# Kernel tuning notes

Measured on AMD Instinct MI355X. Metric: run time of the kernel, lower is better.

The kernel has to match this reference:

```python
import jax, jax.numpy as jnp
import numpy as np

D, S, O, T, B = 32, 8, 4, 256, 1024  # hidden dim, sensory dim, output dim, steps, batch


def setup_inputs() -> dict:
    key = jax.random.key(0)
    ks = iter(jax.random.split(key, 48))

    def w(*shape):
        # stand-in for orthogonal init scaled to max-abs ~0.99
        return jax.random.normal(next(ks), shape, jnp.float32) * 0.17

    inp = {"obs": jax.random.normal(next(ks), (T, B, S), jnp.float32)}
    inp["enc_w"] = w(D, S)
    inp["enc_b"] = jnp.zeros((D,), jnp.float32)
    for name in ["wW", "wI", "wA", "zW", "zI", "zA", "rW", "rI", "rA",
                 "hW", "hI", "hA", "aW", "aI", "aA"]:
        inp[name] = w(D, D)
    for name in ["att", "wmg", "img", "amg"]:
        inp[name + "_w"] = w(D, 2 * D)
        inp[name + "_b"] = jnp.zeros((D,), jnp.float32)
    inp["z_b"] = -jnp.ones((D,), jnp.float32)  # nn.init.constant_(I_z_bias, -1.0)
    inp["r_b"] = jnp.zeros((D,), jnp.float32)
    inp["h_b"] = jnp.zeros((D,), jnp.float32)
    inp["a_b"] = jnp.zeros((D,), jnp.float32)
    inp["phi_w"] = w(O, D)
    inp["phi_b"] = jnp.zeros((O,), jnp.float32)
    return inp


def reference(obs, enc_w, enc_b, wW, wI, wA, att_w, att_b, wmg_w, wmg_b,
              zW, zI, zA, z_b, rW, rI, rA, r_b, hW, hI, hA, h_b,
              img_w, img_b, aW, aI, aA, a_b, amg_w, amg_b, phi_w, phi_b):
    b, d = obs.shape[1], wW.shape[0]

    def lin(x, w, bias=None):
        y = x @ w.T
        return y + bias if bias is not None else y

    def step(carry, o_t):
        W, I, A = carry
        obs_enc = jnp.tanh(lin(o_t, enc_w, enc_b))
        W_all = lin(W, wW) + lin(I, wI) + lin(A, wA)
        attn = jax.nn.sigmoid(lin(jnp.concatenate([W, I], -1), att_w, att_b))
        mult = jax.nn.sigmoid(lin(jnp.concatenate([I, A], -1), wmg_w, wmg_b))
        W_new = jnp.tanh(obs_enc * attn + W_all * mult)
        z = jax.nn.sigmoid(lin(W_new, zW) + lin(I, zI) + lin(A, zA) + z_b)
        r = jax.nn.sigmoid(lin(W_new, rW) + lin(I, rI) + lin(A, rA) + r_b)
        h = jnp.tanh(lin(W_new, hW) + lin(r * I, hI) + lin(A, hA) + h_b)
        mult_I = jax.nn.sigmoid(lin(jnp.concatenate([W_new, A], -1), img_w, img_b))
        I_new = (1 - z) * I + z * (h * mult_I)
        A_all = lin(W_new, aW) + lin(I_new, aI) + lin(A, aA) + a_b
        mult_A = jax.nn.sigmoid(lin(jnp.concatenate([W_new, I_new], -1), amg_w, amg_b))
        A_new = jnp.tanh(A_all * mult_A)
        return (W_new, I_new, A_new), lin(A_new, phi_w, phi_b)

    z0 = jnp.zeros((b, d), obs.dtype)
    _, actions = jax.lax.scan(step, (z0, z0, z0), obs)
    return actions  # [T, B, O]
```

## Files before the change

kernel.cpp:

```cpp
#include <hip/hip_runtime.h>
#include <hip/hip_bf16.h>

typedef __attribute__((ext_vector_type(4))) float f32x4;
typedef __attribute__((ext_vector_type(8))) short s16x8;
typedef __attribute__((ext_vector_type(2))) unsigned int u32x2;
typedef __attribute__((ext_vector_type(4))) unsigned int u32x4;

#define DEV static __device__ __forceinline__

constexpr int Tn = 256, Bn = 1024, Sn = 8;
constexpr float L2E   =  1.44269504f;
constexpr float NL2E  = -1.44269504f;
constexpr float N2L2E = -2.88539008f;

struct Params {
  const float* obs; const float* enc_w; const float* enc_b;
  const float* mw[15];
  const float* gw[4];
  const float* gb[4];
  const float* z_b; const float* r_b; const float* h_b; const float* a_b;
  const float* phi_w; const float* phi_b;
  float* out;
};

DEV f32x4 ld4(const float* p) { return *(const f32x4*)p; }
DEV f32x4 zero4() { f32x4 r = {0.f,0.f,0.f,0.f}; return r; }
DEV s16x8 zero8() { s16x8 r = {0,0,0,0,0,0,0,0}; return r; }

DEV unsigned cvtpk(float a, float b) {
  __hip_bfloat162 t = __float22bfloat162_rn(make_float2(a, b));
  unsigned u; __builtin_memcpy(&u, &t, 4);
  return u;
}

DEV s16x8 pk2s(f32x4 a, f32x4 b, float s) {
  u32x4 f;
  f[0] = cvtpk(a[0]*s, a[1]*s); f[1] = cvtpk(a[2]*s, a[3]*s);
  f[2] = cvtpk(b[0]*s, b[1]*s); f[3] = cvtpk(b[2]*s, b[3]*s);
  s16x8 r; __builtin_memcpy(&r, &f, 16);
  return r;
}

DEV s16x8 wfrag(const float* w, int row, int ldk, int kofs, int h, float s) {
  const float* p = w + row*ldk + kofs + 4*h;
  return pk2s(ld4(p), ld4(p+16), s);
}

DEV f32x4 MF(s16x8 a, s16x8 b, f32x4 c) {
  return __builtin_amdgcn_mfma_f32_16x16x32_bf16(a, b, c, 0, 0, 0);
}

DEV float ex2(float x)  { return __builtin_amdgcn_exp2f(x); }
DEV float rcp_(float x) { return __builtin_amdgcn_rcpf(x); }
DEV float sg(float a) { return rcp_(1.f + ex2(a)); }
DEV float th(float a) { return fmaf(rcp_(1.f + ex2(a)), 2.f, -1.f); }

DEV unsigned long long pack64(u32x2 v) {
  return ((unsigned long long)v[1] << 32) | v[0];
}
DEV u32x2 unpack64(unsigned long long x) {
  u32x2 r; r[0] = (unsigned)x; r[1] = (unsigned)(x >> 32); return r;
}
DEV u32x2 pkx(f32x4 v) {
  u32x2 r; r[0] = cvtpk(v[0], v[1]); r[1] = cvtpk(v[2], v[3]); return r;
}
DEV s16x8 frag(u32x2 own, u32x2 oth, int wv) {
  u32x4 f;
  if (wv == 0) { f[0]=own[0]; f[1]=own[1]; f[2]=oth[0]; f[3]=oth[1]; }
  else         { f[0]=oth[0]; f[1]=oth[1]; f[2]=own[0]; f[3]=own[1]; }
  s16x8 r; __builtin_memcpy(&r, &f, 16);
  return r;
}

DEV f32x4 scl4(f32x4 v, float s) { f32x4 r; r[0]=v[0]*s; r[1]=v[1]*s; r[2]=v[2]*s; r[3]=v[3]*s; return r; }

__global__ __launch_bounds__(128, 1) void anima_kernel(Params P) {
  const int tid  = threadIdx.x;
  const int wv   = tid >> 6;
  const int lane = tid & 63;
  const int h = lane >> 4, c = lane & 15;
  const int bbase = blockIdx.x * 16;
  const int row = wv*16 + c;

  __shared__ unsigned long long xb[4][128];

  const float msc[15] = {N2L2E,N2L2E,N2L2E,  NL2E,NL2E,NL2E,  NL2E,NL2E,NL2E,
                         N2L2E,N2L2E,N2L2E,  N2L2E,N2L2E,N2L2E};
  s16x8 m[15];
#pragma unroll
  for (int i = 0; i < 15; ++i) m[i] = wfrag(P.mw[i], row, 32, 0, h, msc[i]);

  s16x8 g[4][2];
#pragma unroll
  for (int i = 0; i < 4; ++i)
#pragma unroll
    for (int q = 0; q < 2; ++q)
      g[i][q] = wfrag(P.gw[i], row, 64, 32*q, h, NL2E);

  s16x8 ef = zero8();
  if (h < 2) { f32x4 v = ld4(P.enc_w + row*Sn + 4*h); ef = pk2s(v, zero4(), N2L2E); }

  s16x8 pf = (wv == 0 && c < 4) ? wfrag(P.phi_w, c, 32, 0, h, 1.0f) : zero8();

  const int o = wv*16 + 4*h;
  f32x4 bE  = scl4(ld4(P.enc_b + o), N2L2E);
  f32x4 bAt = scl4(ld4(P.gb[0] + o), NL2E);
  f32x4 bMu = scl4(ld4(P.gb[1] + o), NL2E);
  f32x4 bMI = scl4(ld4(P.gb[2] + o), NL2E);
  f32x4 bMA = scl4(ld4(P.gb[3] + o), NL2E);
  f32x4 bZ  = scl4(ld4(P.z_b + o),  NL2E);
  f32x4 bR  = scl4(ld4(P.r_b + o),  NL2E);
  f32x4 bH  = scl4(ld4(P.h_b + o),  N2L2E);
  f32x4 bA  = scl4(ld4(P.a_b + o),  N2L2E);
  f32x4 pb  = (wv == 0 && h == 0) ? ld4(P.phi_b) : zero4();

  f32x4 iv = zero4();
  s16x8 Wf = zero8(), If = zero8(), Af = zero8();

  f32x4 ob = zero4();
  if (h < 2) ob = ld4(P.obs + (size_t)(bbase + c) * Sn + 4*h);

#pragma unroll 1
  for (int t = 0; t < Tn; ++t) {
    s16x8 Of = (h < 2) ? pk2s(ob, zero4(), 1.0f) : zero8();
    f32x4 nb = ob;
    if (h < 2 && t + 1 < Tn)
      nb = ld4(P.obs + ((size_t)(t+1)*Bn + bbase + c) * Sn + 4*h);

    f32x4 x = MF(m[0], Wf, zero4()); x = MF(m[1], If, x); f32x4 aWl = MF(m[2], Af, x);
    f32x4 y = MF(g[0][0], Wf, bAt);  f32x4 aAt = MF(g[0][1], If, y);
    f32x4 u = MF(g[1][0], If, bMu);  f32x4 aMu = MF(g[1][1], Af, u);
    f32x4 aE = MF(ef, Of, bE);
    f32x4 wn;
#pragma unroll
    for (int r = 0; r < 4; ++r) {
      float etp = fmaf(rcp_(1.f + ex2(aE[r])), -4.f*L2E, 2.f*L2E);
      float at  = sg(aAt[r]);
      float mg  = sg(aMu[r]);
      float wp  = fmaf(etp, at, aWl[r]*mg);
      wn[r] = th(wp);
    }
    u32x2 wn2 = pkx(wn);
    xb[0][tid] = pack64(wn2); __syncthreads();
    s16x8 Wnf = frag(wn2, unpack64(xb[0][tid ^ 64]), wv);

    x = MF(m[3], Wnf, bZ); x = MF(m[4], If, x); f32x4 aZ = MF(m[5], Af, x);
    y = MF(m[6], Wnf, bR); y = MF(m[7], If, y); f32x4 aR = MF(m[8], Af, y);
    u = MF(g[2][0], Wnf, bMI); f32x4 aMI = MF(g[2][1], Af, u);
    f32x4 zz, ri, mi;
#pragma unroll
    for (int r = 0; r < 4; ++r) {
      zz[r] = sg(aZ[r]);
      ri[r] = sg(aR[r]) * iv[r];
      mi[r] = sg(aMI[r]);
    }
    u32x2 ri2 = pkx(ri);
    xb[1][tid] = pack64(ri2); __syncthreads();
    s16x8 rIf = frag(ri2, unpack64(xb[1][tid ^ 64]), wv);

    x = MF(m[9], Wnf, bH); x = MF(m[10], rIf, x); f32x4 aH = MF(m[11], Af, x);
    f32x4 inw;
#pragma unroll
    for (int r = 0; r < 4; ++r) {
      float hv = th(aH[r]);
      float tt = hv * mi[r];
      inw[r] = fmaf(zz[r], tt - iv[r], iv[r]);
    }
    u32x2 in2 = pkx(inw);
    xb[2][tid] = pack64(in2); __syncthreads();
    s16x8 Inf = frag(in2, unpack64(xb[2][tid ^ 64]), wv);

    x = MF(m[12], Wnf, bA); x = MF(m[13], Inf, x); f32x4 aAl = MF(m[14], Af, x);
    y = MF(g[3][0], Wnf, bMA); f32x4 aMA = MF(g[3][1], Inf, y);
    f32x4 an;
#pragma unroll
    for (int r = 0; r < 4; ++r) {
      float ma = sg(aMA[r]);
      an[r] = th(aAl[r] * ma);
    }
    u32x2 an2 = pkx(an);
    xb[3][tid] = pack64(an2); __syncthreads();
    s16x8 Anf = frag(an2, unpack64(xb[3][tid ^ 64]), wv);

    if (wv == 0) {
      f32x4 aP = MF(pf, Anf, pb);
      if (h == 0)
        *(f32x4*)(P.out + ((size_t)t*Bn + bbase + c) * 4) = aP;
    }

    Wf = Wnf; If = Inf; Af = Anf; iv = inw; ob = nb;
  }
}

extern "C" void kernel_launch(void* const* d_in, const int* in_sizes, int n_in,
                              void* d_out, int out_size, void* d_ws, size_t ws_size,
                              hipStream_t stream) {
  (void)in_sizes; (void)n_in; (void)d_ws; (void)ws_size; (void)out_size;
  Params p;
  p.obs   = (const float*)d_in[0];
  p.enc_w = (const float*)d_in[1];
  p.enc_b = (const float*)d_in[2];
  for (int i = 0; i < 15; ++i) p.mw[i] = (const float*)d_in[3 + i];
  for (int i = 0; i < 4; ++i) {
    p.gw[i] = (const float*)d_in[18 + 2*i];
    p.gb[i] = (const float*)d_in[19 + 2*i];
  }
  p.z_b   = (const float*)d_in[26];
  p.r_b   = (const float*)d_in[27];
  p.h_b   = (const float*)d_in[28];
  p.a_b   = (const float*)d_in[29];
  p.phi_w = (const float*)d_in[30];
  p.phi_b = (const float*)d_in[31];
  p.out   = (float*)d_out;

  hipLaunchKernelGGL(anima_kernel, dim3(Bn / 16), dim3(128), 0, stream, p);
}
```

Before: 412.3 us.

## Interleave two batch tiles per block to overlap independent recurrence chains

Each block now processes two independent 16-row batch tiles and interleaves their MFMA chains and activations within every phase, sharing the four barriers per step. The goal is to hide MFMA and transcendental latency in the serial recurrence through instruction-level parallelism. It halves the number of blocks, leaving more CUs idle, and doubles the register state per thread.

```diff
diff --git a/kernel.cpp b/kernel.cpp
--- a/kernel.cpp
+++ b/kernel.cpp
@@ -79,10 +79,10 @@
   const int wv   = tid >> 6;
   const int lane = tid & 63;
   const int h = lane >> 4, c = lane & 15;
-  const int bbase = blockIdx.x * 16;
+  const int bbase = blockIdx.x * 32;
   const int row = wv*16 + c;
 
-  __shared__ unsigned long long xb[4][128];
+  __shared__ unsigned long long xb[4][2][128];
 
   const float msc[15] = {N2L2E,N2L2E,N2L2E,  NL2E,NL2E,NL2E,  NL2E,NL2E,NL2E,
                          N2L2E,N2L2E,N2L2E,  N2L2E,N2L2E,N2L2E};
@@ -114,81 +114,141 @@
   f32x4 bA  = scl4(ld4(P.a_b + o),  N2L2E);
   f32x4 pb  = (wv == 0 && h == 0) ? ld4(P.phi_b) : zero4();
 
-  f32x4 iv = zero4();
-  s16x8 Wf = zero8(), If = zero8(), Af = zero8();
-
-  f32x4 ob = zero4();
-  if (h < 2) ob = ld4(P.obs + (size_t)(bbase + c) * Sn + 4*h);
+  f32x4 iv[2]; s16x8 Wf[2], If[2], Af[2]; f32x4 ob[2];
+#pragma unroll
+  for (int q = 0; q < 2; ++q) {
+    iv[q] = zero4(); Wf[q] = zero8(); If[q] = zero8(); Af[q] = zero8();
+    ob[q] = zero4();
+    if (h < 2) ob[q] = ld4(P.obs + (size_t)(bbase + q*16 + c) * Sn + 4*h);
+  }
 
 #pragma unroll 1
   for (int t = 0; t < Tn; ++t) {
-    s16x8 Of = (h < 2) ? pk2s(ob, zero4(), 1.0f) : zero8();
-    f32x4 nb = ob;
-    if (h < 2 && t + 1 < Tn)
-      nb = ld4(P.obs + ((size_t)(t+1)*Bn + bbase + c) * Sn + 4*h);
-
-    f32x4 x = MF(m[0], Wf, zero4()); x = MF(m[1], If, x); f32x4 aWl = MF(m[2], Af, x);
-    f32x4 y = MF(g[0][0], Wf, bAt);  f32x4 aAt = MF(g[0][1], If, y);
-    f32x4 u = MF(g[1][0], If, bMu);  f32x4 aMu = MF(g[1][1], Af, u);
-    f32x4 aE = MF(ef, Of, bE);
-    f32x4 wn;
-#pragma unroll
-    for (int r = 0; r < 4; ++r) {
-      float etp = fmaf(rcp_(1.f + ex2(aE[r])), -4.f*L2E, 2.f*L2E);
-      float at  = sg(aAt[r]);
-      float mg  = sg(aMu[r]);
-      float wp  = fmaf(etp, at, aWl[r]*mg);
-      wn[r] = th(wp);
-    }
-    u32x2 wn2 = pkx(wn);
-    xb[0][tid] = pack64(wn2); __syncthreads();
-    s16x8 Wnf = frag(wn2, unpack64(xb[0][tid ^ 64]), wv);
-
-    x = MF(m[3], Wnf, bZ); x = MF(m[4], If, x); f32x4 aZ = MF(m[5], Af, x);
-    y = MF(m[6], Wnf, bR); y = MF(m[7], If, y); f32x4 aR = MF(m[8], Af, y);
-    u = MF(g[2][0], Wnf, bMI); f32x4 aMI = MF(g[2][1], Af, u);
-    f32x4 zz, ri, mi;
-#pragma unroll
-    for (int r = 0; r < 4; ++r) {
-      zz[r] = sg(aZ[r]);
-      ri[r] = sg(aR[r]) * iv[r];
-      mi[r] = sg(aMI[r]);
-    }
-    u32x2 ri2 = pkx(ri);
-    xb[1][tid] = pack64(ri2); __syncthreads();
-    s16x8 rIf = frag(ri2, unpack64(xb[1][tid ^ 64]), wv);
-
-    x = MF(m[9], Wnf, bH); x = MF(m[10], rIf, x); f32x4 aH = MF(m[11], Af, x);
-    f32x4 inw;
-#pragma unroll
-    for (int r = 0; r < 4; ++r) {
-      float hv = th(aH[r]);
-      float tt = hv * mi[r];
-      inw[r] = fmaf(zz[r], tt - iv[r], iv[r]);
-    }
-    u32x2 in2 = pkx(inw);
-    xb[2][tid] = pack64(in2); __syncthreads();
-    s16x8 Inf = frag(in2, unpack64(xb[2][tid ^ 64]), wv);
-
-    x = MF(m[12], Wnf, bA); x = MF(m[13], Inf, x); f32x4 aAl = MF(m[14], Af, x);
-    y = MF(g[3][0], Wnf, bMA); f32x4 aMA = MF(g[3][1], Inf, y);
-    f32x4 an;
-#pragma unroll
-    for (int r = 0; r < 4; ++r) {
-      float ma = sg(aMA[r]);
-      an[r] = th(aAl[r] * ma);
-    }
-    u32x2 an2 = pkx(an);
-    xb[3][tid] = pack64(an2); __syncthreads();
-    s16x8 Anf = frag(an2, unpack64(xb[3][tid ^ 64]), wv);
+    s16x8 Of[2]; f32x4 nb[2];
+#pragma unroll
+    for (int q = 0; q < 2; ++q) {
+      Of[q] = (h < 2) ? pk2s(ob[q], zero4(), 1.0f) : zero8();
+      nb[q] = ob[q];
+      if (h < 2 && t + 1 < Tn)
+        nb[q] = ld4(P.obs + ((size_t)(t+1)*Bn + bbase + q*16 + c) * Sn + 4*h);
+    }
+
+    s16x8 Wnf[2];
+    {
+      f32x4 aWl[2], aAt[2], aMu[2], aE[2];
+#pragma unroll
+      for (int q = 0; q < 2; ++q) {
+        f32x4 x = MF(m[0], Wf[q], zero4()); x = MF(m[1], If[q], x); aWl[q] = MF(m[2], Af[q], x);
+        f32x4 y = MF(g[0][0], Wf[q], bAt);  aAt[q] = MF(g[0][1], If[q], y);
+        f32x4 u = MF(g[1][0], If[q], bMu);  aMu[q] = MF(g[1][1], Af[q], u);
+        aE[q]  = MF(ef, Of[q], bE);
+      }
+      u32x2 wn2[2];
+#pragma unroll
+      for (int q = 0; q < 2; ++q) {
+        f32x4 wn;
+#pragma unroll
+        for (int r = 0; r < 4; ++r) {
+          float etp = fmaf(rcp_(1.f + ex2(aE[q][r])), -4.f*L2E, 2.f*L2E);
+          float at  = sg(aAt[q][r]);
+          float mg  = sg(aMu[q][r]);
+          float wp  = fmaf(etp, at, aWl[q][r]*mg);
+          wn[r] = th(wp);
+        }
+        wn2[q] = pkx(wn);
+        xb[0][q][tid] = pack64(wn2[q]);
+      }
+      __syncthreads();
+#pragma unroll
+      for (int q = 0; q < 2; ++q) Wnf[q] = frag(wn2[q], unpack64(xb[0][q][tid ^ 64]), wv);
+    }
+
+    f32x4 zz[2], mi[2]; s16x8 rIf[2];
+    {
+      f32x4 aZ[2], aR[2], aMI[2];
+#pragma unroll
+      for (int q = 0; q < 2; ++q) {
+        f32x4 x = MF(m[3], Wnf[q], bZ); x = MF(m[4], If[q], x); aZ[q] = MF(m[5], Af[q], x);
+        f32x4 y = MF(m[6], Wnf[q], bR); y = MF(m[7], If[q], y); aR[q] = MF(m[8], Af[q], y);
+        f32x4 u = MF(g[2][0], Wnf[q], bMI); aMI[q] = MF(g[2][1], Af[q], u);
+      }
+      u32x2 ri2[2];
+#pragma unroll
+      for (int q = 0; q < 2; ++q) {
+        f32x4 ri;
+#pragma unroll
+        for (int r = 0; r < 4; ++r) {
+          zz[q][r] = sg(aZ[q][r]);
+          ri[r]    = sg(aR[q][r]) * iv[q][r];
+          mi[q][r] = sg(aMI[q][r]);
+        }
+        ri2[q] = pkx(ri);
+        xb[1][q][tid] = pack64(ri2[q]);
+      }
+      __syncthreads();
+#pragma unroll
+      for (int q = 0; q < 2; ++q) rIf[q] = frag(ri2[q], unpack64(xb[1][q][tid ^ 64]), wv);
+    }
+
+    f32x4 inw[2]; s16x8 Inf[2];
+    {
+      f32x4 aH[2];
+#pragma unroll
+      for (int q = 0; q < 2; ++q) {
+        f32x4 x = MF(m[9], Wnf[q], bH); x = MF(m[10], rIf[q], x); aH[q] = MF(m[11], Af[q], x);
+      }
+      u32x2 in2[2];
+#pragma unroll
+      for (int q = 0; q < 2; ++q) {
+#pragma unroll
+        for (int r = 0; r < 4; ++r) {
+          float hv = th(aH[q][r]);
+          float tt = hv * mi[q][r];
+          inw[q][r] = fmaf(zz[q][r], tt - iv[q][r], iv[q][r]);
+        }
+        in2[q] = pkx(inw[q]);
+        xb[2][q][tid] = pack64(in2[q]);
+      }
+      __syncthreads();
+#pragma unroll
+      for (int q = 0; q < 2; ++q) Inf[q] = frag(in2[q], unpack64(xb[2][q][tid ^ 64]), wv);
+    }
+
+    s16x8 Anf[2];
+    {
+      f32x4 aAl[2], aMA[2];
+#pragma unroll
+      for (int q = 0; q < 2; ++q) {
+        f32x4 x = MF(m[12], Wnf[q], bA); x = MF(m[13], Inf[q], x); aAl[q] = MF(m[14], Af[q], x);
+        f32x4 y = MF(g[3][0], Wnf[q], bMA); aMA[q] = MF(g[3][1], Inf[q], y);
+      }
+      u32x2 an2[2];
+#pragma unroll
+      for (int q = 0; q < 2; ++q) {
+        f32x4 an;
+#pragma unroll
+        for (int r = 0; r < 4; ++r) an[r] = th(aAl[q][r] * sg(aMA[q][r]));
+        an2[q] = pkx(an);
+        xb[3][q][tid] = pack64(an2[q]);
+      }
+      __syncthreads();
+#pragma unroll
+      for (int q = 0; q < 2; ++q) Anf[q] = frag(an2[q], unpack64(xb[3][q][tid ^ 64]), wv);
+    }
 
     if (wv == 0) {
-      f32x4 aP = MF(pf, Anf, pb);
-      if (h == 0)
-        *(f32x4*)(P.out + ((size_t)t*Bn + bbase + c) * 4) = aP;
-    }
-
-    Wf = Wnf; If = Inf; Af = Anf; iv = inw; ob = nb;
+#pragma unroll
+      for (int q = 0; q < 2; ++q) {
+        f32x4 aP = MF(pf, Anf[q], pb);
+        if (h == 0)
+          *(f32x4*)(P.out + ((size_t)t*Bn + bbase + q*16 + c) * 4) = aP;
+      }
+    }
+
+#pragma unroll
+    for (int q = 0; q < 2; ++q) {
+      Wf[q] = Wnf[q]; If[q] = Inf[q]; Af[q] = Anf[q]; iv[q] = inw[q]; ob[q] = nb[q];
+    }
   }
 }
 
@@ -213,5 +273,5 @@
   p.phi_b = (const float*)d_in[31];
   p.out   = (float*)d_out;
 
-  hipLaunchKernelGGL(anima_kernel, dim3(Bn / 16), dim3(128), 0, stream, p);
-}
+  hipLaunchKernelGGL(anima_kernel, dim3(Bn / 32), dim3(128), 0, stream, p);
+}
```

After: 636.6 us. 1.54x slower.

## Reorder recurrent step so MFMAs on ready operands overlap barrier exchanges

Applied to the files above, without the earlier changes.

Restructures the time loop so partial matrix products whose inputs are already known (terms on A, I, W_new) are issued before the shared-memory exchange completes and before the fragment is rebuilt. Work for the next step's W-gate products is hoisted into the tail of the current step, and the output projection is deferred to the following iteration. Observation loads are prefetched two steps ahead. The aim is to shorten the serial dependency chain per step by hiding MFMA latency behind barriers, at the cost of more live registers and a peeled final output.

```diff
diff --git a/kernel.cpp b/kernel.cpp
--- a/kernel.cpp
+++ b/kernel.cpp
@@ -115,38 +115,51 @@
   f32x4 pb  = (wv == 0 && h == 0) ? ld4(P.phi_b) : zero4();
 
   f32x4 iv = zero4();
-  s16x8 Wf = zero8(), If = zero8(), Af = zero8();
-
-  f32x4 ob = zero4();
-  if (h < 2) ob = ld4(P.obs + (size_t)(bbase + c) * Sn + 4*h);
+  s16x8 Inf = zero8();
+  u32x2 an2; an2[0] = 0u; an2[1] = 0u;
+
+  f32x4 ob = zero4(), obN = zero4();
+  if (h < 2) ob  = ld4(P.obs + (size_t)(bbase + c) * Sn + 4*h);
+  if (h < 2) obN = ld4(P.obs + ((size_t)1*Bn + bbase + c) * Sn + 4*h);
+  s16x8 Of = (h < 2) ? pk2s(ob, zero4(), 1.0f) : zero8();
+
+  f32x4 tA1 = zero4();
+  f32x4 yAt = bAt;
+  f32x4 uMu = bMu;
+  f32x4 aE  = MF(ef, Of, bE);
+
+  xb[3][tid] = pack64(an2);
+  __syncthreads();
+  unsigned long long pw3 = xb[3][tid ^ 64];
 
 #pragma unroll 1
   for (int t = 0; t < Tn; ++t) {
-    s16x8 Of = (h < 2) ? pk2s(ob, zero4(), 1.0f) : zero8();
-    f32x4 nb = ob;
-    if (h < 2 && t + 1 < Tn)
-      nb = ld4(P.obs + ((size_t)(t+1)*Bn + bbase + c) * Sn + 4*h);
-
-    f32x4 x = MF(m[0], Wf, zero4()); x = MF(m[1], If, x); f32x4 aWl = MF(m[2], Af, x);
-    f32x4 y = MF(g[0][0], Wf, bAt);  f32x4 aAt = MF(g[0][1], If, y);
-    f32x4 u = MF(g[1][0], If, bMu);  f32x4 aMu = MF(g[1][1], Af, u);
-    f32x4 aE = MF(ef, Of, bE);
+    s16x8 Anf = frag(an2, unpack64(pw3), wv);
+    if (wv == 0 && t) {
+      f32x4 aP = MF(pf, Anf, pb);
+      if (h == 0) *(f32x4*)(P.out + ((size_t)(t-1)*Bn + bbase + c) * 4) = aP;
+    }
+    f32x4 aWl = MF(m[2], Anf, tA1);
+    f32x4 aMu = MF(g[1][1], Anf, uMu);
     f32x4 wn;
 #pragma unroll
     for (int r = 0; r < 4; ++r) {
       float etp = fmaf(rcp_(1.f + ex2(aE[r])), -4.f*L2E, 2.f*L2E);
-      float at  = sg(aAt[r]);
+      float at  = sg(yAt[r]);
       float mg  = sg(aMu[r]);
-      float wp  = fmaf(etp, at, aWl[r]*mg);
-      wn[r] = th(wp);
+      wn[r] = th(fmaf(etp, at, aWl[r]*mg));
     }
     u32x2 wn2 = pkx(wn);
-    xb[0][tid] = pack64(wn2); __syncthreads();
-    s16x8 Wnf = frag(wn2, unpack64(xb[0][tid ^ 64]), wv);
-
-    x = MF(m[3], Wnf, bZ); x = MF(m[4], If, x); f32x4 aZ = MF(m[5], Af, x);
-    y = MF(m[6], Wnf, bR); y = MF(m[7], If, y); f32x4 aR = MF(m[8], Af, y);
-    u = MF(g[2][0], Wnf, bMI); f32x4 aMI = MF(g[2][1], Af, u);
+    xb[0][tid] = pack64(wn2);
+    __syncthreads();
+    unsigned long long pw0 = xb[0][tid ^ 64];
+    f32x4 eZ  = MF(m[5], Anf, MF(m[4], Inf, bZ));
+    f32x4 eR  = MF(m[8], Anf, MF(m[7], Inf, bR));
+    f32x4 eMI = MF(g[2][1], Anf, bMI);
+    s16x8 Wnew = frag(wn2, unpack64(pw0), wv);
+    f32x4 aZ  = MF(m[3], Wnew, eZ);
+    f32x4 aR  = MF(m[6], Wnew, eR);
+    f32x4 aMI = MF(g[2][0], Wnew, eMI);
     f32x4 zz, ri, mi;
 #pragma unroll
     for (int r = 0; r < 4; ++r) {
@@ -155,40 +168,50 @@
       mi[r] = sg(aMI[r]);
     }
     u32x2 ri2 = pkx(ri);
-    xb[1][tid] = pack64(ri2); __syncthreads();
-    s16x8 rIf = frag(ri2, unpack64(xb[1][tid ^ 64]), wv);
-
-    x = MF(m[9], Wnf, bH); x = MF(m[10], rIf, x); f32x4 aH = MF(m[11], Af, x);
+    xb[1][tid] = pack64(ri2);
+    __syncthreads();
+    unsigned long long pw1 = xb[1][tid ^ 64];
+    f32x4 eH  = MF(m[11], Anf, MF(m[9],  Wnew, bH));
+    f32x4 eAl = MF(m[14], Anf, MF(m[12], Wnew, bA));
+    f32x4 eMA = MF(g[3][0], Wnew, bMA);
+    s16x8 rIf = frag(ri2, unpack64(pw1), wv);
+    f32x4 aH = MF(m[10], rIf, eH);
     f32x4 inw;
 #pragma unroll
     for (int r = 0; r < 4; ++r) {
       float hv = th(aH[r]);
-      float tt = hv * mi[r];
-      inw[r] = fmaf(zz[r], tt - iv[r], iv[r]);
+      inw[r] = fmaf(zz[r], hv * mi[r] - iv[r], iv[r]);
     }
     u32x2 in2 = pkx(inw);
-    xb[2][tid] = pack64(in2); __syncthreads();
-    s16x8 Inf = frag(in2, unpack64(xb[2][tid ^ 64]), wv);
-
-    x = MF(m[12], Wnf, bA); x = MF(m[13], Inf, x); f32x4 aAl = MF(m[14], Af, x);
-    y = MF(g[3][0], Wnf, bMA); f32x4 aMA = MF(g[3][1], Inf, y);
+    xb[2][tid] = pack64(in2);
+    __syncthreads();
+    unsigned long long pw2 = xb[2][tid ^ 64];
+    f32x4 t0 = MF(m[0], Wnew, zero4());
+    f32x4 y0 = MF(g[0][0], Wnew, bAt);
+    s16x8 OfN = (h < 2) ? pk2s(obN, zero4(), 1.0f) : zero8();
+    aE = MF(ef, OfN, bE);
+    s16x8 Inew = frag(in2, unpack64(pw2), wv);
+    f32x4 aAl = MF(m[13], Inew, eAl);
+    f32x4 aMA = MF(g[3][1], Inew, eMA);
     f32x4 an;
 #pragma unroll
-    for (int r = 0; r < 4; ++r) {
-      float ma = sg(aMA[r]);
-      an[r] = th(aAl[r] * ma);
-    }
-    u32x2 an2 = pkx(an);
-    xb[3][tid] = pack64(an2); __syncthreads();
-    s16x8 Anf = frag(an2, unpack64(xb[3][tid ^ 64]), wv);
-
-    if (wv == 0) {
-      f32x4 aP = MF(pf, Anf, pb);
-      if (h == 0)
-        *(f32x4*)(P.out + ((size_t)t*Bn + bbase + c) * 4) = aP;
-    }
-
-    Wf = Wnf; If = Inf; Af = Anf; iv = inw; ob = nb;
+    for (int r = 0; r < 4; ++r) an[r] = th(aAl[r] * sg(aMA[r]));
+    an2 = pkx(an);
+    xb[3][tid] = pack64(an2);
+    __syncthreads();
+    pw3 = xb[3][tid ^ 64];
+    tA1 = MF(m[1], Inew, t0);
+    yAt = MF(g[0][1], Inew, y0);
+    uMu = MF(g[1][0], Inew, bMu);
+    if (h < 2 && t + 2 < Tn)
+      obN = ld4(P.obs + ((size_t)(t+2)*Bn + bbase + c) * Sn + 4*h);
+    Inf = Inew; iv = inw;
+  }
+
+  s16x8 Anf = frag(an2, unpack64(pw3), wv);
+  if (wv == 0) {
+    f32x4 aP = MF(pf, Anf, pb);
+    if (h == 0) *(f32x4*)(P.out + ((size_t)(Tn-1)*Bn + bbase + c) * 4) = aP;
   }
 }
 
```

Result: faster. 390.2 us (-5.4%).

## Interleave two batch tiles per block and hoist off-critical-path MFMAs across barriers

Applied to the files above, without the earlier changes.

Each block now processes two independent 16-row batch tiles (A and B) in the same instruction stream, so their MFMA and transcendental chains can fill each other's latency bubbles, and the grid is halved. MFMA terms that do not depend on the freshly exchanged fragment are issued before it is read from shared memory, and next-step partial products, obs encodings and the phi output are moved across iterations as software pipelining. This trades more register pressure and half as many blocks (32 instead of 64, less CU parallelism) for shorter dependent latency per step.

```diff
diff --git a/kernel.cpp b/kernel.cpp
--- a/kernel.cpp
+++ b/kernel.cpp
@@ -79,10 +79,10 @@
   const int wv   = tid >> 6;
   const int lane = tid & 63;
   const int h = lane >> 4, c = lane & 15;
-  const int bbase = blockIdx.x * 16;
+  const int bbase = blockIdx.x * 32;
   const int row = wv*16 + c;
 
-  __shared__ unsigned long long xb[4][128];
+  __shared__ unsigned long long xb[4][2][128];
 
   const float msc[15] = {N2L2E,N2L2E,N2L2E,  NL2E,NL2E,NL2E,  NL2E,NL2E,NL2E,
                          N2L2E,N2L2E,N2L2E,  N2L2E,N2L2E,N2L2E};
@@ -114,81 +114,171 @@
   f32x4 bA  = scl4(ld4(P.a_b + o),  N2L2E);
   f32x4 pb  = (wv == 0 && h == 0) ? ld4(P.phi_b) : zero4();
 
-  f32x4 iv = zero4();
-  s16x8 Wf = zero8(), If = zero8(), Af = zero8();
-
-  f32x4 ob = zero4();
-  if (h < 2) ob = ld4(P.obs + (size_t)(bbase + c) * Sn + 4*h);
+  f32x4 ivA = zero4(), ivB = zero4();
+  s16x8 InfA = zero8(), InfB = zero8();
+  u32x2 an2A; an2A[0]=0u; an2A[1]=0u;
+  u32x2 an2B; an2B[0]=0u; an2B[1]=0u;
+
+  f32x4 obA = zero4(), obB = zero4(), obNA = zero4(), obNB = zero4();
+  if (h < 2) {
+    obA  = ld4(P.obs + (size_t)(bbase + c) * Sn + 4*h);
+    obB  = ld4(P.obs + (size_t)(bbase + 16 + c) * Sn + 4*h);
+    obNA = ld4(P.obs + ((size_t)1*Bn + bbase + c) * Sn + 4*h);
+    obNB = ld4(P.obs + ((size_t)1*Bn + bbase + 16 + c) * Sn + 4*h);
+  }
+  s16x8 OfA = (h < 2) ? pk2s(obA, zero4(), 1.0f) : zero8();
+  s16x8 OfB = (h < 2) ? pk2s(obB, zero4(), 1.0f) : zero8();
+
+  f32x4 tA1A = zero4(), tA1B = zero4();
+  f32x4 yAtA = bAt,     yAtB = bAt;
+  f32x4 uMuA = bMu,     uMuB = bMu;
+  f32x4 aEA  = MF(ef, OfA, bE);
+  f32x4 aEB  = MF(ef, OfB, bE);
+
+  xb[3][0][tid] = pack64(an2A);
+  xb[3][1][tid] = pack64(an2B);
+  __syncthreads();
+  unsigned long long pw3A = xb[3][0][tid ^ 64];
+  unsigned long long pw3B = xb[3][1][tid ^ 64];
 
 #pragma unroll 1
   for (int t = 0; t < Tn; ++t) {
-    s16x8 Of = (h < 2) ? pk2s(ob, zero4(), 1.0f) : zero8();
-    f32x4 nb = ob;
-    if (h < 2 && t + 1 < Tn)
-      nb = ld4(P.obs + ((size_t)(t+1)*Bn + bbase + c) * Sn + 4*h);
-
-    f32x4 x = MF(m[0], Wf, zero4()); x = MF(m[1], If, x); f32x4 aWl = MF(m[2], Af, x);
-    f32x4 y = MF(g[0][0], Wf, bAt);  f32x4 aAt = MF(g[0][1], If, y);
-    f32x4 u = MF(g[1][0], If, bMu);  f32x4 aMu = MF(g[1][1], Af, u);
-    f32x4 aE = MF(ef, Of, bE);
-    f32x4 wn;
+    s16x8 AnfA = frag(an2A, unpack64(pw3A), wv);
+    s16x8 AnfB = frag(an2B, unpack64(pw3B), wv);
+    if (wv == 0 && t) {
+      f32x4 aPA = MF(pf, AnfA, pb);
+      f32x4 aPB = MF(pf, AnfB, pb);
+      if (h == 0) {
+        *(f32x4*)(P.out + ((size_t)(t-1)*Bn + bbase + c) * 4) = aPA;
+        *(f32x4*)(P.out + ((size_t)(t-1)*Bn + bbase + 16 + c) * 4) = aPB;
+      }
+    }
+    f32x4 aWlA = MF(m[2], AnfA, tA1A);
+    f32x4 aWlB = MF(m[2], AnfB, tA1B);
+    f32x4 aMuA = MF(g[1][1], AnfA, uMuA);
+    f32x4 aMuB = MF(g[1][1], AnfB, uMuB);
+    f32x4 wnA, wnB;
 #pragma unroll
     for (int r = 0; r < 4; ++r) {
-      float etp = fmaf(rcp_(1.f + ex2(aE[r])), -4.f*L2E, 2.f*L2E);
-      float at  = sg(aAt[r]);
-      float mg  = sg(aMu[r]);
-      float wp  = fmaf(etp, at, aWl[r]*mg);
-      wn[r] = th(wp);
-    }
-    u32x2 wn2 = pkx(wn);
-    xb[0][tid] = pack64(wn2); __syncthreads();
-    s16x8 Wnf = frag(wn2, unpack64(xb[0][tid ^ 64]), wv);
-
-    x = MF(m[3], Wnf, bZ); x = MF(m[4], If, x); f32x4 aZ = MF(m[5], Af, x);
-    y = MF(m[6], Wnf, bR); y = MF(m[7], If, y); f32x4 aR = MF(m[8], Af, y);
-    u = MF(g[2][0], Wnf, bMI); f32x4 aMI = MF(g[2][1], Af, u);
-    f32x4 zz, ri, mi;
+      float etpA = fmaf(rcp_(1.f + ex2(aEA[r])), -4.f*L2E, 2.f*L2E);
+      float etpB = fmaf(rcp_(1.f + ex2(aEB[r])), -4.f*L2E, 2.f*L2E);
+      float atA  = sg(yAtA[r]);
+      float atB  = sg(yAtB[r]);
+      float mgA  = sg(aMuA[r]);
+      float mgB  = sg(aMuB[r]);
+      wnA[r] = th(fmaf(etpA, atA, aWlA[r]*mgA));
+      wnB[r] = th(fmaf(etpB, atB, aWlB[r]*mgB));
+    }
+    u32x2 wn2A = pkx(wnA);
+    u32x2 wn2B = pkx(wnB);
+    xb[0][0][tid] = pack64(wn2A);
+    xb[0][1][tid] = pack64(wn2B);
+    __syncthreads();
+    unsigned long long pw0A = xb[0][0][tid ^ 64];
+    unsigned long long pw0B = xb[0][1][tid ^ 64];
+    f32x4 eZA  = MF(m[5], AnfA, MF(m[4], InfA, bZ));
+    f32x4 eZB  = MF(m[5], AnfB, MF(m[4], InfB, bZ));
+    f32x4 eRA  = MF(m[8], AnfA, MF(m[7], InfA, bR));
+    f32x4 eRB  = MF(m[8], AnfB, MF(m[7], InfB, bR));
+    f32x4 eMIA = MF(g[2][1], AnfA, bMI);
+    f32x4 eMIB = MF(g[2][1], AnfB, bMI);
+    s16x8 WnewA = frag(wn2A, unpack64(pw0A), wv);
+    s16x8 WnewB = frag(wn2B, unpack64(pw0B), wv);
+    f32x4 aZA  = MF(m[3], WnewA, eZA);
+    f32x4 aZB  = MF(m[3], WnewB, eZB);
+    f32x4 aRA  = MF(m[6], WnewA, eRA);
+    f32x4 aRB  = MF(m[6], WnewB, eRB);
+    f32x4 aMIA = MF(g[2][0], WnewA, eMIA);
+    f32x4 aMIB = MF(g[2][0], WnewB, eMIB);
+    f32x4 zzA, riA, miA, zzB, riB, miB;
 #pragma unroll
     for (int r = 0; r < 4; ++r) {
-      zz[r] = sg(aZ[r]);
-      ri[r] = sg(aR[r]) * iv[r];
-      mi[r] = sg(aMI[r]);
-    }
-    u32x2 ri2 = pkx(ri);
-    xb[1][tid] = pack64(ri2); __syncthreads();
-    s16x8 rIf = frag(ri2, unpack64(xb[1][tid ^ 64]), wv);
-
-    x = MF(m[9], Wnf, bH); x = MF(m[10], rIf, x); f32x4 aH = MF(m[11], Af, x);
-    f32x4 inw;
+      zzA[r] = sg(aZA[r]);        zzB[r] = sg(aZB[r]);
+      riA[r] = sg(aRA[r]) * ivA[r]; riB[r] = sg(aRB[r]) * ivB[r];
+      miA[r] = sg(aMIA[r]);       miB[r] = sg(aMIB[r]);
+    }
+    u32x2 ri2A = pkx(riA);
+    u32x2 ri2B = pkx(riB);
+    xb[1][0][tid] = pack64(ri2A);
+    xb[1][1][tid] = pack64(ri2B);
+    __syncthreads();
+    unsigned long long pw1A = xb[1][0][tid ^ 64];
+    unsigned long long pw1B = xb[1][1][tid ^ 64];
+    f32x4 eHA  = MF(m[11], AnfA, MF(m[9],  WnewA, bH));
+    f32x4 eHB  = MF(m[11], AnfB, MF(m[9],  WnewB, bH));
+    f32x4 eAlA = MF(m[14], AnfA, MF(m[12], WnewA, bA));
+    f32x4 eAlB = MF(m[14], AnfB, MF(m[12], WnewB, bA));
+    f32x4 eMAA = MF(g[3][0], WnewA, bMA);
+    f32x4 eMAB = MF(g[3][0], WnewB, bMA);
+    s16x8 rIfA = frag(ri2A, unpack64(pw1A), wv);
+    s16x8 rIfB = frag(ri2B, unpack64(pw1B), wv);
+    f32x4 aHA = MF(m[10], rIfA, eHA);
+    f32x4 aHB = MF(m[10], rIfB, eHB);
+    f32x4 inwA, inwB;
 #pragma unroll
     for (int r = 0; r < 4; ++r) {
-      float hv = th(aH[r]);
-      float tt = hv * mi[r];
-      inw[r] = fmaf(zz[r], tt - iv[r], iv[r]);
-    }
-    u32x2 in2 = pkx(inw);
-    xb[2][tid] = pack64(in2); __syncthreads();
-    s16x8 Inf = frag(in2, unpack64(xb[2][tid ^ 64]), wv);
-
-    x = MF(m[12], Wnf, bA); x = MF(m[13], Inf, x); f32x4 aAl = MF(m[14], Af, x);
-    y = MF(g[3][0], Wnf, bMA); f32x4 aMA = MF(g[3][1], Inf, y);
-    f32x4 an;
+      float hvA = th(aHA[r]);
+      float hvB = th(aHB[r]);
+      inwA[r] = fmaf(zzA[r], hvA * miA[r] - ivA[r], ivA[r]);
+      inwB[r] = fmaf(zzB[r], hvB * miB[r] - ivB[r], ivB[r]);
+    }
+    u32x2 in2A = pkx(inwA);
+    u32x2 in2B = pkx(inwB);
+    xb[2][0][tid] = pack64(in2A);
+    xb[2][1][tid] = pack64(in2B);
+    __syncthreads();
+    unsigned long long pw2A = xb[2][0][tid ^ 64];
+    unsigned long long pw2B = xb[2][1][tid ^ 64];
+    f32x4 t0A = MF(m[0], WnewA, zero4());
+    f32x4 t0B = MF(m[0], WnewB, zero4());
+    f32x4 y0A = MF(g[0][0], WnewA, bAt);
+    f32x4 y0B = MF(g[0][0], WnewB, bAt);
+    s16x8 OfNA = (h < 2) ? pk2s(obNA, zero4(), 1.0f) : zero8();
+    s16x8 OfNB = (h < 2) ? pk2s(obNB, zero4(), 1.0f) : zero8();
+    aEA = MF(ef, OfNA, bE);
+    aEB = MF(ef, OfNB, bE);
+    s16x8 InewA = frag(in2A, unpack64(pw2A), wv);
+    s16x8 InewB = frag(in2B, unpack64(pw2B), wv);
+    f32x4 aAlA = MF(m[13], InewA, eAlA);
+    f32x4 aAlB = MF(m[13], InewB, eAlB);
+    f32x4 aMAA = MF(g[3][1], InewA, eMAA);
+    f32x4 aMAB = MF(g[3][1], InewB, eMAB);
+    f32x4 anA, anB;
 #pragma unroll
     for (int r = 0; r < 4; ++r) {
-      float ma = sg(aMA[r]);
-      an[r] = th(aAl[r] * ma);
-    }
-    u32x2 an2 = pkx(an);
-    xb[3][tid] = pack64(an2); __syncthreads();
-    s16x8 Anf = frag(an2, unpack64(xb[3][tid ^ 64]), wv);
-
-    if (wv == 0) {
-      f32x4 aP = MF(pf, Anf, pb);
-      if (h == 0)
-        *(f32x4*)(P.out + ((size_t)t*Bn + bbase + c) * 4) = aP;
-    }
-
-    Wf = Wnf; If = Inf; Af = Anf; iv = inw; ob = nb;
+      anA[r] = th(aAlA[r] * sg(aMAA[r]));
+      anB[r] = th(aAlB[r] * sg(aMAB[r]));
+    }
+    an2A = pkx(anA);
+    an2B = pkx(anB);
+    xb[3][0][tid] = pack64(an2A);
+    xb[3][1][tid] = pack64(an2B);
+    __syncthreads();
+    pw3A = xb[3][0][tid ^ 64];
+    pw3B = xb[3][1][tid ^ 64];
+    tA1A = MF(m[1], InewA, t0A);
+    tA1B = MF(m[1], InewB, t0B);
+    yAtA = MF(g[0][1], InewA, y0A);
+    yAtB = MF(g[0][1], InewB, y0B);
+    uMuA = MF(g[1][0], InewA, bMu);
+    uMuB = MF(g[1][0], InewB, bMu);
+    if (h < 2 && t + 2 < Tn) {
+      obNA = ld4(P.obs + ((size_t)(t+2)*Bn + bbase + c) * Sn + 4*h);
+      obNB = ld4(P.obs + ((size_t)(t+2)*Bn + bbase + 16 + c) * Sn + 4*h);
+    }
+    InfA = InewA; ivA = inwA;
+    InfB = InewB; ivB = inwB;
+  }
+
+  s16x8 AnfA = frag(an2A, unpack64(pw3A), wv);
+  s16x8 AnfB = frag(an2B, unpack64(pw3B), wv);
+  if (wv == 0) {
+    f32x4 aPA = MF(pf, AnfA, pb);
+    f32x4 aPB = MF(pf, AnfB, pb);
+    if (h == 0) {
+      *(f32x4*)(P.out + ((size_t)(Tn-1)*Bn + bbase + c) * 4) = aPA;
+      *(f32x4*)(P.out + ((size_t)(Tn-1)*Bn + bbase + 16 + c) * 4) = aPB;
+    }
   }
 }
 
@@ -213,5 +303,5 @@
   p.phi_b = (const float*)d_in[31];
   p.out   = (float*)d_out;
 
-  hipLaunchKernelGGL(anima_kernel, dim3(Bn / 16), dim3(128), 0, stream, p);
-}
+  hipLaunchKernelGGL(anima_kernel, dim3(Bn / 32), dim3(128), 0, stream, p);
+}
```

Result: slower. 562.0 us (+36.3%).
